# Optimization experiments

Measured on AMD Instinct MI355X. Metric: run time of the kernel, lower is better.

The kernel has to match this reference:

```python
import math
import jax, jax.numpy as jnp
import numpy as np

B, T, D, H = 2, 2048, 1024, 16
HD = D // H
LN_EPS = 1e-5


def new_gelu(x):
    c = math.sqrt(2.0 / math.pi)
    return 0.5 * x * (1.0 + jnp.tanh(c * (x + 0.044715 * x * x * x)))


def layer_norm(x, w, b):
    mu = jnp.mean(x, axis=-1, keepdims=True)
    var = jnp.var(x, axis=-1, keepdims=True)
    return (x - mu) * jax.lax.rsqrt(var + LN_EPS) * w + b


def setup_inputs() -> dict:
    key = jax.random.key(0)
    ks = jax.random.split(key, 9)
    s = 0.02
    return {
        "x": jax.random.normal(ks[0], (B, T, D), jnp.float32),
        "wq": jax.random.normal(ks[1], (D, D), jnp.float32) * s,
        "wk": jax.random.normal(ks[2], (D, D), jnp.float32) * s,
        "wv": jax.random.normal(ks[3], (D, D), jnp.float32) * s,
        "Er": jax.random.normal(ks[4], (H, T, HD), jnp.float32),
        "fc1_w": jax.random.normal(ks[5], (4 * D, D), jnp.float32) * s,
        "fc1_b": jax.random.normal(ks[6], (4 * D,), jnp.float32) * s,
        "fc2_w": jax.random.normal(ks[7], (D, 4 * D), jnp.float32) * s,
        "fc2_b": jax.random.normal(ks[8], (D,), jnp.float32) * s,
        "ln1_w": jnp.ones((D,), jnp.float32),
        "ln1_b": jnp.zeros((D,), jnp.float32),
        "ln2_w": jnp.ones((D,), jnp.float32),
        "ln2_b": jnp.zeros((D,), jnp.float32),
    }


def rel_attention(x, wq, wk, wv, Er):
    b, t, c = x.shape
    # torch nn.Linear: y = x @ W^T  (weights stored [out, in])
    q = (x @ wq.T).reshape(b, t, H, HD).transpose(0, 2, 1, 3)  # [B,H,T,HD]
    k = (x @ wk.T).reshape(b, t, H, HD).transpose(0, 2, 1, 3)
    v = (x @ wv.T).reshape(b, t, H, HD).transpose(0, 2, 1, 3)

    raw_attn = jnp.einsum("bhqd,bhkd->bhqk", q, k)  # [B,H,T,T]
    # relative-position logits + skew trick
    srel = jnp.einsum("bhqd,hrd->bhqr", q, Er[:, -t:, :])  # [B,H,T,T]
    srel = jnp.pad(srel, ((0, 0), (0, 0), (0, 0), (1, 0)))  # [B,H,T,T+1]
    srel = srel.reshape(b, H, t + 1, t)[:, :, 1:, :]  # skewed [B,H,T,T]

    attn = (raw_attn + srel) * (1.0 / math.sqrt(HD))
    causal = jnp.tril(jnp.ones((t, t), bool))
    attn = jnp.where(causal[None, None], attn, -jnp.inf)
    attn = jax.nn.softmax(attn, axis=-1)

    y = jnp.einsum("bhqk,bhkd->bhqd", attn, v)
    return y.transpose(0, 2, 1, 3).reshape(b, t, c)


def reference(x, wq, wk, wv, Er, fc1_w, fc1_b, fc2_w, fc2_b, ln1_w, ln1_b, ln2_w, ln2_b):
    x = x + rel_attention(layer_norm(x, ln1_w, ln1_b), wq, wk, wv, Er)
    h = layer_norm(x, ln2_w, ln2_b)
    h = new_gelu(h @ fc1_w.T + fc1_b)
    x = x + (h @ fc2_w.T + fc2_b)
    return x
```

## Files before the change

kernel.cpp:

```cpp
#include <hip/hip_runtime.h>
#include <hip/hip_bf16.h>

#define Bb 2
#define Tt 2048
#define Dd 1024
#define Hh 16

typedef short s16x8 __attribute__((ext_vector_type(8)));
typedef float f32x4 __attribute__((ext_vector_type(4)));
typedef unsigned short u16;
typedef short mfma_in_t __attribute__((ext_vector_type(8)));

typedef const __attribute__((address_space(1))) void gvoid;
typedef __attribute__((address_space(3))) void lvoid;

__device__ inline u16 f2bf(float f) {
  union { float f; unsigned u; } v; v.f = f;
  unsigned r = v.u + 0x7FFF + ((v.u >> 16) & 1);
  return (u16)(r >> 16);
}
__device__ inline float bf2f(u16 v) {
  return __builtin_bit_cast(float, (unsigned)v << 16);
}

__device__ inline f32x4 MFMA(s16x8 a, s16x8 b, f32x4 c) {
  return __builtin_amdgcn_mfma_f32_16x16x32_bf16(
      __builtin_bit_cast(mfma_in_t, a), __builtin_bit_cast(mfma_in_t, b), c, 0, 0, 0);
}

__global__ __launch_bounds__(256) void ln_kernel(const float* __restrict__ x,
    const float* __restrict__ w, const float* __restrict__ b, u16* __restrict__ out) {
  int row = blockIdx.x;
  const float4 v = ((const float4*)(x + (size_t)row * Dd))[threadIdx.x];
  float s = v.x + v.y + v.z + v.w;
  float sq = v.x * v.x + v.y * v.y + v.z * v.z + v.w * v.w;
#pragma unroll
  for (int off = 32; off; off >>= 1) { s += __shfl_down(s, off); sq += __shfl_down(sq, off); }
  __shared__ float red[8];
  int wid = threadIdx.x >> 6;
  if ((threadIdx.x & 63) == 0) { red[wid] = s; red[4 + wid] = sq; }
  __syncthreads();
  s = red[0] + red[1] + red[2] + red[3];
  sq = red[4] + red[5] + red[6] + red[7];
  float mean = s * (1.0f / Dd);
  float var = sq * (1.0f / Dd) - mean * mean;
  float rs = rsqrtf(var + 1e-5f);
  float4 wv = ((const float4*)w)[threadIdx.x];
  float4 bv = ((const float4*)b)[threadIdx.x];
  ushort4 o = make_ushort4(f2bf((v.x - mean) * rs * wv.x + bv.x),
                           f2bf((v.y - mean) * rs * wv.y + bv.y),
                           f2bf((v.z - mean) * rs * wv.z + bv.z),
                           f2bf((v.w - mean) * rs * wv.w + bv.w));
  ((ushort4*)(out + (size_t)row * Dd))[threadIdx.x] = o;
}

__global__ __launch_bounds__(256) void cvt_kernel(const float* __restrict__ in, u16* __restrict__ out) {
  int i = blockIdx.x * 256 + threadIdx.x;
  const float4* p = (const float4*)in;
  float4 a = p[i * 2], b2 = p[i * 2 + 1];
  ((ushort4*)out)[i * 2]     = make_ushort4(f2bf(a.x), f2bf(a.y), f2bf(a.z), f2bf(a.w));
  ((ushort4*)out)[i * 2 + 1] = make_ushort4(f2bf(b2.x), f2bf(b2.y), f2bf(b2.z), f2bf(b2.w));
}

__global__ __launch_bounds__(256) void vtrans_kernel(const u16* __restrict__ qkv, u16* __restrict__ vt) {
  __shared__ u16 L[64 * 72];
  const int tok0 = blockIdx.x * 64, h = blockIdx.y, b = blockIdx.z;
  const int t = threadIdx.x;
#pragma unroll
  for (int i = 0; i < 2; i++) {
    int f = i * 256 + t;
    int row = f >> 3, ch = f & 7;
    *(s16x8*)&L[row * 72 + ch * 8] =
        *(const s16x8*)(qkv + (size_t)(b * Tt + tok0 + row) * 3072 + 2 * Dd + h * 64 + ch * 8);
  }
  __syncthreads();
#pragma unroll
  for (int i = 0; i < 2; i++) {
    int f = i * 256 + t;
    int d = f & 63, c = f >> 6;
    s16x8 o;
#pragma unroll
    for (int e = 0; e < 8; e++) o[e] = (short)L[(c * 8 + e) * 72 + d];
    *(s16x8*)(vt + ((size_t)(b * Hh + h) * 64 + d) * Tt + tok0 + c * 8) = o;
  }
}

template <int EPI, int BN>
__global__ __launch_bounds__(256) void gemm_bt(
    const u16* __restrict__ A, const u16* __restrict__ W,
    const float* __restrict__ bias, const float* __restrict__ res,
    void* __restrict__ outp, int K, int ldout) {
  constexpr int MR = (BN == 128) ? 4 : 2;
  __shared__ u16 As[2][128 * 32];
  __shared__ u16 Bs[2][BN * 32];
  const int bm = blockIdx.x, bn = blockIdx.y;
  const int t = threadIdx.x, lane = t & 63, w = t >> 6;
  const int l15 = lane & 15, l16 = lane >> 4;
  const int rbase = (BN == 128) ? (w >> 1) * 64 : w * 32;
  const int cbase = (BN == 128) ? (w & 1) * 64 : 0;
  f32x4 acc[MR][4] = {};
  const u16* Abase = A + (size_t)(bm * 128) * K;
  const u16* Wbase = W + (size_t)(bn * BN) * K;
  const int frow = lane >> 2;
  const int fcol = ((lane & 3) ^ (frow & 3)) * 8;
#define GEMM_STAGE(k0_, nb_)                                                              \
  _Pragma("unroll")                                                                       \
  for (int i = 0; i < 2; i++) {                                                           \
    int q = w * 2 + i;                                                                    \
    int row = q * 16 + frow;                                                              \
    __builtin_amdgcn_global_load_lds((gvoid*)(Abase + (size_t)row * K + (k0_) + fcol),    \
                                     (lvoid*)&As[nb_][q * 512], 16, 0, 0);                \
    if (BN == 128 || i == 0) {                                                            \
      int qb2 = (BN == 128) ? q : w;                                                      \
      int rowb = qb2 * 16 + frow;                                                         \
      __builtin_amdgcn_global_load_lds((gvoid*)(Wbase + (size_t)rowb * K + (k0_) + fcol), \
                                       (lvoid*)&Bs[nb_][qb2 * 512], 16, 0, 0);            \
    }                                                                                     \
  }
  GEMM_STAGE(0, 0);
  __syncthreads();
  int cur = 0;
  for (int k0 = 0; k0 < K; k0 += 32) {
    if (k0 + 32 < K) { GEMM_STAGE(k0 + 32, cur ^ 1); }
    s16x8 af[MR], bfr[4];
#pragma unroll
    for (int rt = 0; rt < MR; rt++) {
      int ar = rbase + rt * 16 + l15;
      af[rt] = *(const s16x8*)&As[cur][ar * 32 + (l16 ^ (ar & 3)) * 8];
    }
#pragma unroll
    for (int ct = 0; ct < 4; ct++) {
      int br = cbase + ct * 16 + l15;
      bfr[ct] = *(const s16x8*)&Bs[cur][br * 32 + (l16 ^ (br & 3)) * 8];
    }
#pragma unroll
    for (int rt = 0; rt < MR; rt++)
#pragma unroll
      for (int ct = 0; ct < 4; ct++)
        acc[rt][ct] = MFMA(af[rt], bfr[ct], acc[rt][ct]);
    __syncthreads();
    cur ^= 1;
  }
  const int rg0 = bm * 128 + rbase + l16 * 4;
  const int cg0 = bn * BN + cbase + l15;
#pragma unroll
  for (int rt = 0; rt < MR; rt++) {
#pragma unroll
    for (int ct = 0; ct < 4; ct++) {
#pragma unroll
      for (int j = 0; j < 4; j++) {
        int r = rg0 + rt * 16 + j;
        int c = cg0 + ct * 16;
        float v = acc[rt][ct][j];
        if constexpr (EPI == 0) {
          ((u16*)outp)[(size_t)r * ldout + c] = f2bf(v);
        } else if constexpr (EPI == 1) {
          v += bias[c];
          float u = 0.7978845608f * (v + 0.044715f * v * v * v);
          float th = 1.0f - 2.0f / (__expf(2.0f * u) + 1.0f);
          ((u16*)outp)[(size_t)r * ldout + c] = f2bf(0.5f * v * (1.0f + th));
        } else {
          v += bias[c] + res[(size_t)r * Dd + c];
          ((float*)outp)[(size_t)r * ldout + c] = v;
        }
      }
    }
  }
}

__global__ __launch_bounds__(256, 2) void attn_kernel(
    const u16* __restrict__ qkv,
    const u16* __restrict__ erb,
    const u16* __restrict__ vt,
    const float* __restrict__ x,
    float* __restrict__ x2) {
  __shared__ u16 Ksm[64 * 72];
  __shared__ u16 Vsm[64 * 72];
  __shared__ u16 Esm[128 * 72];
  __shared__ u16 Gsm[4][16 * 82];
  const int h = blockIdx.y, b = blockIdx.z;
  const int t = threadIdx.x, lane = t & 63, w = t >> 6;
  const int l15 = lane & 15, l16 = lane >> 4;
  u16* gw = Gsm[w];
  u16* Pw = gw;
  const int tr = t >> 3, tc = (t & 7) * 8;
  const u16* kbase = qkv + ((size_t)b * Tt) * 3072 + Dd + h * 64;
  const u16* vbase = vt + ((size_t)(b * Hh + h) * 64) * Tt;
  const u16* ebase = erb + (size_t)h * Tt * 64;
  s16x8 kR0, kR1, vR0, vR1, eR0, eR1, eR2, eR3;
#define ATTN_PREFETCH(kjn_, qin_)                                              \
  {                                                                            \
    const int kjn = (kjn_);                                                    \
    kR0 = *(const s16x8*)(kbase + (size_t)(kjn + tr) * 3072 + tc);             \
    kR1 = *(const s16x8*)(kbase + (size_t)(kjn + 32 + tr) * 3072 + tc);        \
    vR0 = *(const s16x8*)(vbase + (size_t)tr * Tt + kjn + tc);                 \
    vR1 = *(const s16x8*)(vbase + (size_t)(32 + tr) * Tt + kjn + tc);          \
    const int rlo = Tt - 64 - (qin_) + kjn;                                    \
    int g0 = rlo + tr;          g0 = g0 > Tt - 1 ? Tt - 1 : g0;                \
    int g1 = rlo + 32 + tr;     g1 = g1 > Tt - 1 ? Tt - 1 : g1;                \
    int g2 = rlo + 64 + tr;     g2 = g2 > Tt - 1 ? Tt - 1 : g2;                \
    int g3 = rlo + 96 + tr;     g3 = g3 > Tt - 1 ? Tt - 1 : g3;                \
    eR0 = *(const s16x8*)(ebase + (size_t)g0 * 64 + tc);                       \
    eR1 = *(const s16x8*)(ebase + (size_t)g1 * 64 + tc);                       \
    eR2 = *(const s16x8*)(ebase + (size_t)g2 * 64 + tc);                       \
    eR3 = *(const s16x8*)(ebase + (size_t)g3 * 64 + tc);                       \
  }
  for (int pass = 0; pass < 2; ++pass) {
    const int qt = pass ? 31 - (int)blockIdx.x : (int)blockIdx.x;
    const int qi = qt * 64;
    const int nt = qt + 1;
    const int qb = qi + w * 16;
    const u16* qp = qkv + (size_t)(b * Tt + qb + l15) * 3072 + h * 64 + l16 * 8;
    const s16x8 qf0 = *(const s16x8*)qp;
    const s16x8 qf1 = *(const s16x8*)(qp + 32);
    f32x4 o_acc[4] = {};
    float l_lane[4] = {0.f, 0.f, 0.f, 0.f};
    if (pass == 0) { ATTN_PREFETCH(0, qi); }
    for (int it = 0; it < nt; ++it) {
      const int kj = it * 64;
      *(s16x8*)&Ksm[tr * 72 + tc] = kR0;
      *(s16x8*)&Ksm[(32 + tr) * 72 + tc] = kR1;
      *(s16x8*)&Vsm[tr * 72 + tc] = vR0;
      *(s16x8*)&Vsm[(32 + tr) * 72 + tc] = vR1;
      *(s16x8*)&Esm[tr * 72 + tc] = eR0;
      *(s16x8*)&Esm[(32 + tr) * 72 + tc] = eR1;
      *(s16x8*)&Esm[(64 + tr) * 72 + tc] = eR2;
      *(s16x8*)&Esm[(96 + tr) * 72 + tc] = eR3;
      __syncthreads();
      if (it + 1 < nt) {
        ATTN_PREFETCH(kj + 64, qi);
      } else if (pass == 0) {
        ATTN_PREFETCH(0, (31 - (int)blockIdx.x) * 64);
      }
      f32x4 s_acc[4] = {};
#pragma unroll
      for (int ct = 0; ct < 4; ct++) {
        int col = ct * 16 + l15;
        s16x8 k0 = *(const s16x8*)&Ksm[col * 72 + l16 * 8];
        s16x8 k1 = *(const s16x8*)&Ksm[col * 72 + 32 + l16 * 8];
        s_acc[ct] = MFMA(qf1, k1, MFMA(qf0, k0, s_acc[ct]));
      }
      const int ub = 48 - 16 * w;
#pragma unroll
      for (int gt = 0; gt < 5; gt++) {
        int ur = ub + gt * 16 + l15;
        s16x8 e0 = *(const s16x8*)&Esm[ur * 72 + l16 * 8];
        s16x8 e1 = *(const s16x8*)&Esm[ur * 72 + 32 + l16 * 8];
        f32x4 z = {};
        f32x4 ga = MFMA(qf1, e1, MFMA(qf0, e0, z));
#pragma unroll
        for (int j = 0; j < 4; j++) gw[(l16 * 4 + j) * 82 + gt * 16 + l15] = f2bf(ga[j]);
      }
      float p[4][4];
      if (kj + 63 <= qb) {
#pragma unroll
        for (int j = 0; j < 4; j++) {
          const int di = l16 * 4 + j;
          float lacc = 0.f;
#pragma unroll
          for (int ct = 0; ct < 4; ct++) {
            int dj = ct * 16 + l15;
            float pe = __expf((s_acc[ct][j] + bf2f(gw[di * 82 + dj - di + 15])) * 0.125f - 8.0f);
            p[j][ct] = pe;
            lacc += pe;
          }
          l_lane[j] += lacc;
        }
      } else {
#pragma unroll
        for (int j = 0; j < 4; j++) {
          const int di = l16 * 4 + j;
          const int ig = qb + di;
          float lacc = 0.f;
#pragma unroll
          for (int ct = 0; ct < 4; ct++) {
            int dj = ct * 16 + l15;
            float pe = 0.f;
            if (kj + dj <= ig)
              pe = __expf((s_acc[ct][j] + bf2f(gw[di * 82 + dj - di + 15])) * 0.125f - 8.0f);
            p[j][ct] = pe;
            lacc += pe;
          }
          l_lane[j] += lacc;
        }
      }
#pragma unroll
      for (int j = 0; j < 4; j++)
#pragma unroll
        for (int ct = 0; ct < 4; ct++)
          Pw[(l16 * 4 + j) * 72 + ct * 16 + l15] = f2bf(p[j][ct]);
      s16x8 pa0 = *(const s16x8*)&Pw[l15 * 72 + l16 * 8];
      s16x8 pa1 = *(const s16x8*)&Pw[l15 * 72 + 32 + l16 * 8];
#pragma unroll
      for (int g = 0; g < 4; g++) {
        s16x8 v0 = *(const s16x8*)&Vsm[(g * 16 + l15) * 72 + l16 * 8];
        s16x8 v1 = *(const s16x8*)&Vsm[(g * 16 + l15) * 72 + 32 + l16 * 8];
        o_acc[g] = MFMA(pa1, v1, MFMA(pa0, v0, o_acc[g]));
      }
      __syncthreads();
    }
#pragma unroll
    for (int j = 0; j < 4; j++) {
#pragma unroll
      for (int o = 1; o < 16; o <<= 1) l_lane[j] += __shfl_xor(l_lane[j], o);
    }
#pragma unroll
    for (int g = 0; g < 4; g++)
#pragma unroll
      for (int j = 0; j < 4; j++) {
        int r = qb + l16 * 4 + j;
        int c = h * 64 + g * 16 + l15;
        size_t idx = (size_t)(b * Tt + r) * Dd + c;
        x2[idx] = x[idx] + o_acc[g][j] / l_lane[j];
      }
  }
}

extern "C" void kernel_launch(void* const* d_in, const int* in_sizes, int n_in,
                              void* d_out, int out_size, void* d_ws, size_t ws_size,
                              hipStream_t stream) {
  const float* x     = (const float*)d_in[0];
  const float* wq    = (const float*)d_in[1];
  const float* wk    = (const float*)d_in[2];
  const float* wv    = (const float*)d_in[3];
  const float* Er    = (const float*)d_in[4];
  const float* fc1_w = (const float*)d_in[5];
  const float* fc1_b = (const float*)d_in[6];
  const float* fc2_w = (const float*)d_in[7];
  const float* fc2_b = (const float*)d_in[8];
  const float* ln1_w = (const float*)d_in[9];
  const float* ln1_b = (const float*)d_in[10];
  const float* ln2_w = (const float*)d_in[11];
  const float* ln2_b = (const float*)d_in[12];

  const size_t MB = 1024 * 1024;
  char* ws = (char*)d_ws;
  u16*   h1   = (u16*)ws;
  u16*   qkv  = (u16*)(ws + 8 * MB);
  u16*   vtb  = (u16*)(ws + 32 * MB);
  u16*   erb  = (u16*)(ws + 40 * MB);
  float* x2   = (float*)(ws + 44 * MB);
  u16*   wqkb = (u16*)(ws + 60 * MB);
  u16*   f1b  = (u16*)(ws + 66 * MB);
  u16*   f2b  = (u16*)(ws + 74 * MB);
  u16*   a1   = (u16*)(ws + 8 * MB);
  float* out  = (float*)d_out;

  ln_kernel<<<dim3(Bb * Tt), 256, 0, stream>>>(x, ln1_w, ln1_b, h1);
  cvt_kernel<<<dim3(1024), 256, 0, stream>>>(Er, erb);
  cvt_kernel<<<dim3(512), 256, 0, stream>>>(wq, wqkb);
  cvt_kernel<<<dim3(512), 256, 0, stream>>>(wk, wqkb + 1024 * 1024);
  cvt_kernel<<<dim3(512), 256, 0, stream>>>(wv, wqkb + 2 * 1024 * 1024);
  cvt_kernel<<<dim3(2048), 256, 0, stream>>>(fc1_w, f1b);
  cvt_kernel<<<dim3(2048), 256, 0, stream>>>(fc2_w, f2b);
  gemm_bt<0, 128><<<dim3(32, 24), 256, 0, stream>>>(h1, wqkb, nullptr, nullptr, qkv, Dd, 3072);
  vtrans_kernel<<<dim3(32, 16, 2), 256, 0, stream>>>(qkv, vtb);
  attn_kernel<<<dim3(16, 16, 2), 256, 0, stream>>>(qkv, erb, vtb, x, x2);
  ln_kernel<<<dim3(Bb * Tt), 256, 0, stream>>>(x2, ln2_w, ln2_b, h1);
  gemm_bt<1, 128><<<dim3(32, 32), 256, 0, stream>>>(h1, f1b, fc1_b, nullptr, a1, Dd, 4096);
  gemm_bt<2, 64><<<dim3(32, 16), 256, 0, stream>>>(a1, f2b, fc2_b, x2, out, 4096, Dd);
}
```

Baseline: 276.7 us.

## Merge weight conversions into one launch, pad attention LDS, add setprio hints

Replaces six separate fp32-to-bf16 conversion launches with a single kernel that picks its source and destination from the block index, cutting per-launch overhead. Changes the LDS row strides of the attention scratch buffers (82 to 85 for the rel-pos gather, 72 to 68 for P) to alter the bank-conflict pattern. Raises wave priority around the MFMA sections of attention and adds a two-blocks-per-CU occupancy hint to the GEMM. The GEMM launch-bounds hint may force register spills, and the new strides may not suit the 16-byte vector reads.

Result: faster. 267.0 us (-3.5%).

```diff
diff --git a/kernel.cpp b/kernel.cpp
--- a/kernel.cpp
+++ b/kernel.cpp
@@ -54,12 +54,26 @@
   ((ushort4*)(out + (size_t)row * Dd))[threadIdx.x] = o;
 }
 
-__global__ __launch_bounds__(256) void cvt_kernel(const float* __restrict__ in, u16* __restrict__ out) {
-  int i = blockIdx.x * 256 + threadIdx.x;
-  const float4* p = (const float4*)in;
+__global__ __launch_bounds__(256) void cvt6_kernel(
+    const float* __restrict__ s0, u16* __restrict__ d0,
+    const float* __restrict__ s1, u16* __restrict__ d1,
+    const float* __restrict__ s2, u16* __restrict__ d2,
+    const float* __restrict__ s3, u16* __restrict__ d3,
+    const float* __restrict__ s4, u16* __restrict__ d4,
+    const float* __restrict__ s5, u16* __restrict__ d5) {
+  int blk = blockIdx.x;
+  const float* s; u16* d; int base;
+  if (blk < 1024)      { s = s0; d = d0; base = blk; }
+  else if (blk < 1536) { s = s1; d = d1; base = blk - 1024; }
+  else if (blk < 2048) { s = s2; d = d2; base = blk - 1536; }
+  else if (blk < 2560) { s = s3; d = d3; base = blk - 2048; }
+  else if (blk < 4608) { s = s4; d = d4; base = blk - 2560; }
+  else                 { s = s5; d = d5; base = blk - 4608; }
+  int i = base * 256 + threadIdx.x;
+  const float4* p = (const float4*)s;
   float4 a = p[i * 2], b2 = p[i * 2 + 1];
-  ((ushort4*)out)[i * 2]     = make_ushort4(f2bf(a.x), f2bf(a.y), f2bf(a.z), f2bf(a.w));
-  ((ushort4*)out)[i * 2 + 1] = make_ushort4(f2bf(b2.x), f2bf(b2.y), f2bf(b2.z), f2bf(b2.w));
+  ((ushort4*)d)[i * 2]     = make_ushort4(f2bf(a.x), f2bf(a.y), f2bf(a.z), f2bf(a.w));
+  ((ushort4*)d)[i * 2 + 1] = make_ushort4(f2bf(b2.x), f2bf(b2.y), f2bf(b2.z), f2bf(b2.w));
 }
 
 __global__ __launch_bounds__(256) void vtrans_kernel(const u16* __restrict__ qkv, u16* __restrict__ vt) {
@@ -86,7 +100,7 @@
 }
 
 template <int EPI, int BN>
-__global__ __launch_bounds__(256) void gemm_bt(
+__global__ __launch_bounds__(256, 2) void gemm_bt(
     const u16* __restrict__ A, const u16* __restrict__ W,
     const float* __restrict__ bias, const float* __restrict__ res,
     void* __restrict__ outp, int K, int ldout) {
@@ -177,7 +191,7 @@
   __shared__ u16 Ksm[64 * 72];
   __shared__ u16 Vsm[64 * 72];
   __shared__ u16 Esm[128 * 72];
-  __shared__ u16 Gsm[4][16 * 82];
+  __shared__ u16 Gsm[4][16 * 85];
   const int h = blockIdx.y, b = blockIdx.z;
   const int t = threadIdx.x, lane = t & 63, w = t >> 6;
   const int l15 = lane & 15, l16 = lane >> 4;
@@ -232,6 +246,7 @@
       } else if (pass == 0) {
         ATTN_PREFETCH(0, (31 - (int)blockIdx.x) * 64);
       }
+      __builtin_amdgcn_s_setprio(1);
       f32x4 s_acc[4] = {};
 #pragma unroll
       for (int ct = 0; ct < 4; ct++) {
@@ -249,8 +264,9 @@
         f32x4 z = {};
         f32x4 ga = MFMA(qf1, e1, MFMA(qf0, e0, z));
 #pragma unroll
-        for (int j = 0; j < 4; j++) gw[(l16 * 4 + j) * 82 + gt * 16 + l15] = f2bf(ga[j]);
-      }
+        for (int j = 0; j < 4; j++) gw[(l16 * 4 + j) * 85 + gt * 16 + l15] = f2bf(ga[j]);
+      }
+      __builtin_amdgcn_s_setprio(0);
       float p[4][4];
       if (kj + 63 <= qb) {
 #pragma unroll
@@ -260,7 +276,7 @@
 #pragma unroll
           for (int ct = 0; ct < 4; ct++) {
             int dj = ct * 16 + l15;
-            float pe = __expf((s_acc[ct][j] + bf2f(gw[di * 82 + dj - di + 15])) * 0.125f - 8.0f);
+            float pe = __expf((s_acc[ct][j] + bf2f(gw[di * 85 + dj - di + 15])) * 0.125f - 8.0f);
             p[j][ct] = pe;
             lacc += pe;
           }
@@ -277,7 +293,7 @@
             int dj = ct * 16 + l15;
             float pe = 0.f;
             if (kj + dj <= ig)
-              pe = __expf((s_acc[ct][j] + bf2f(gw[di * 82 + dj - di + 15])) * 0.125f - 8.0f);
+              pe = __expf((s_acc[ct][j] + bf2f(gw[di * 85 + dj - di + 15])) * 0.125f - 8.0f);
             p[j][ct] = pe;
             lacc += pe;
           }
@@ -288,15 +304,17 @@
       for (int j = 0; j < 4; j++)
 #pragma unroll
         for (int ct = 0; ct < 4; ct++)
-          Pw[(l16 * 4 + j) * 72 + ct * 16 + l15] = f2bf(p[j][ct]);
-      s16x8 pa0 = *(const s16x8*)&Pw[l15 * 72 + l16 * 8];
-      s16x8 pa1 = *(const s16x8*)&Pw[l15 * 72 + 32 + l16 * 8];
+          Pw[(l16 * 4 + j) * 68 + ct * 16 + l15] = f2bf(p[j][ct]);
+      s16x8 pa0 = *(const s16x8*)&Pw[l15 * 68 + l16 * 8];
+      s16x8 pa1 = *(const s16x8*)&Pw[l15 * 68 + 32 + l16 * 8];
+      __builtin_amdgcn_s_setprio(1);
 #pragma unroll
       for (int g = 0; g < 4; g++) {
         s16x8 v0 = *(const s16x8*)&Vsm[(g * 16 + l15) * 72 + l16 * 8];
         s16x8 v1 = *(const s16x8*)&Vsm[(g * 16 + l15) * 72 + 32 + l16 * 8];
         o_acc[g] = MFMA(pa1, v1, MFMA(pa0, v0, o_acc[g]));
       }
+      __builtin_amdgcn_s_setprio(0);
       __syncthreads();
     }
 #pragma unroll
@@ -347,12 +365,9 @@
   float* out  = (float*)d_out;
 
   ln_kernel<<<dim3(Bb * Tt), 256, 0, stream>>>(x, ln1_w, ln1_b, h1);
-  cvt_kernel<<<dim3(1024), 256, 0, stream>>>(Er, erb);
-  cvt_kernel<<<dim3(512), 256, 0, stream>>>(wq, wqkb);
-  cvt_kernel<<<dim3(512), 256, 0, stream>>>(wk, wqkb + 1024 * 1024);
-  cvt_kernel<<<dim3(512), 256, 0, stream>>>(wv, wqkb + 2 * 1024 * 1024);
-  cvt_kernel<<<dim3(2048), 256, 0, stream>>>(fc1_w, f1b);
-  cvt_kernel<<<dim3(2048), 256, 0, stream>>>(fc2_w, f2b);
+  cvt6_kernel<<<dim3(6656), 256, 0, stream>>>(
+      Er, erb, wq, wqkb, wk, wqkb + 1024 * 1024, wv, wqkb + 2 * 1024 * 1024,
+      fc1_w, f1b, fc2_w, f2b);
   gemm_bt<0, 128><<<dim3(32, 24), 256, 0, stream>>>(h1, wqkb, nullptr, nullptr, qkv, Dd, 3072);
   vtrans_kernel<<<dim3(32, 16, 2), 256, 0, stream>>>(qkv, vtb);
   attn_kernel<<<dim3(16, 16, 2), 256, 0, stream>>>(qkv, erb, vtb, x, x2);
```
